# Kernel tuning notes

Hardware: AMD Instinct MI355X
Metric: run time of the kernel (lower is better)

## Reference

```python
import jax, jax.numpy as jnp
import numpy as np

N_RAYS = 65536   # 256x256 image
N_PTS = 128      # samples per ray
FEAT = 3         # RGB
FAR_DELTA = 1e10 # sentinel delta for last sample, as in the torch module


def setup_inputs() -> dict:
    key = jax.random.key(0)
    k1, k2, k3 = jax.random.split(key, 3)
    # depths along each ray must be increasing (deltas computed by diff)
    depth_values = jnp.sort(
        jax.random.uniform(k1, (N_RAYS, N_PTS), jnp.float32, 2.0, 6.0), axis=-1)
    density = jax.random.uniform(k2, (N_RAYS, N_PTS), jnp.float32)  # non-negative
    feature = jax.random.uniform(k3, (N_RAYS, N_PTS, FEAT), jnp.float32)
    return {"depth_values": depth_values, "density": density, "feature": feature}


def reference(depth_values, density, feature):
    n_rays, n_pts = depth_values.shape
    # deltas: consecutive depth differences, huge value appended for last bin
    deltas = jnp.concatenate(
        [depth_values[:, 1:] - depth_values[:, :-1],
         jnp.full((n_rays, 1), FAR_DELTA, depth_values.dtype)], axis=-1)
    tau = density * deltas                              # [n_rays, n_pts]
    # transmittance T_i = exp(-sum_{j<i} tau_j) (exclusive cumsum in log space)
    log_T = -jnp.concatenate(
        [jnp.zeros((n_rays, 1), tau.dtype), jnp.cumsum(tau[:, :-1], axis=-1)],
        axis=-1)
    weights = jnp.exp(log_T) * (1.0 - jnp.exp(-tau))    # [n_rays, n_pts]
    feat_out = jnp.einsum('np,npf->nf', weights, feature)         # [n_rays, F]
    depth_out = jnp.sum(weights * depth_values, axis=-1, keepdims=True)
    return jnp.concatenate([feat_out, depth_out], axis=-1)        # [n_rays, F+1]
```

## Files before the change

kernel.cpp:

```cpp
#include <hip/hip_runtime.h>

#define N_RAYS 65536
#define N_PTS 128
#define FEAT 3
#define FAR_DELTA 1e10f

__global__ __launch_bounds__(256) void volrend_kernel(
    const float* __restrict__ depth,
    const float* __restrict__ density,
    const float* __restrict__ feature,
    float* __restrict__ out)
{
    const int wave = threadIdx.x >> 6;
    const int lane = threadIdx.x & 63;
    const int seg  = lane >> 5;
    const int s    = lane & 31;
    const int base = (blockIdx.x * 4 + wave) * 4;

    const int rayA = base + seg;
    const int rayB = base + 2 + seg;

    const float4 dA = *(const float4*)(depth   + rayA * N_PTS + 4 * s);
    const float4 rA = *(const float4*)(density + rayA * N_PTS + 4 * s);
    const float4 dB = *(const float4*)(depth   + rayB * N_PTS + 4 * s);
    const float4 rB = *(const float4*)(density + rayB * N_PTS + 4 * s);
    const float4* fA = (const float4*)(feature + (size_t)rayA * (N_PTS * FEAT)) + 3 * s;
    const float4* fB = (const float4*)(feature + (size_t)rayB * (N_PTS * FEAT)) + 3 * s;
    const float4 fA0 = fA[0], fA1 = fA[1], fA2 = fA[2];
    const float4 fB0 = fB[0], fB1 = fB[1], fB2 = fB[2];

    float nxA = __shfl_down(dA.x, 1);
    float nxB = __shfl_down(dB.x, 1);
    const bool last = (s == 31);
    float tA0 = rA.x * (dA.y - dA.x);
    float tA1 = rA.y * (dA.z - dA.y);
    float tA2 = rA.z * (dA.w - dA.z);
    float tA3 = rA.w * (last ? FAR_DELTA : (nxA - dA.w));
    float tB0 = rB.x * (dB.y - dB.x);
    float tB1 = rB.y * (dB.z - dB.y);
    float tB2 = rB.z * (dB.w - dB.z);
    float tB3 = rB.w * (last ? FAR_DELTA : (nxB - dB.w));

    float pA = tA0 + tA1 + tA2 + tA3;
    float pB = tB0 + tB1 + tB2 + tB3;
    float eA = __shfl_up(pA, 1, 32);
    float eB = __shfl_up(pB, 1, 32);
    if (s == 0) { eA = 0.0f; eB = 0.0f; }
    #pragma unroll
    for (int off = 1; off < 32; off <<= 1) {
        float xA = __shfl_up(eA, off, 32);
        float xB = __shfl_up(eB, off, 32);
        if (s >= off) { eA += xA; eB += xB; }
    }

    float TA0 = __expf(-eA);
    float TA1 = __expf(-(eA + tA0));
    float TA2 = __expf(-(eA + tA0 + tA1));
    float TA3 = __expf(-(eA + tA0 + tA1 + tA2));
    float TA4 = __expf(-(eA + pA));
    float TB0 = __expf(-eB);
    float TB1 = __expf(-(eB + tB0));
    float TB2 = __expf(-(eB + tB0 + tB1));
    float TB3 = __expf(-(eB + tB0 + tB1 + tB2));
    float TB4 = __expf(-(eB + pB));
    float wA0 = TA0 - TA1, wA1 = TA1 - TA2, wA2 = TA2 - TA3, wA3 = TA3 - TA4;
    float wB0 = TB0 - TB1, wB1 = TB1 - TB2, wB2 = TB2 - TB3, wB3 = TB3 - TB4;

    float a0 = wA0 * fA0.x + wA1 * fA0.w + wA2 * fA1.z + wA3 * fA2.y;
    float a1 = wA0 * fA0.y + wA1 * fA1.x + wA2 * fA1.w + wA3 * fA2.z;
    float a2 = wA0 * fA0.z + wA1 * fA1.y + wA2 * fA2.x + wA3 * fA2.w;
    float a3 = wA0 * dA.x  + wA1 * dA.y  + wA2 * dA.z  + wA3 * dA.w;
    float b0 = wB0 * fB0.x + wB1 * fB0.w + wB2 * fB1.z + wB3 * fB2.y;
    float b1 = wB0 * fB0.y + wB1 * fB1.x + wB2 * fB1.w + wB3 * fB2.z;
    float b2 = wB0 * fB0.z + wB1 * fB1.y + wB2 * fB2.x + wB3 * fB2.w;
    float b3 = wB0 * dB.x  + wB1 * dB.y  + wB2 * dB.z  + wB3 * dB.w;

    #pragma unroll
    for (int off = 16; off > 0; off >>= 1) {
        a0 += __shfl_down(a0, off, 32);
        a1 += __shfl_down(a1, off, 32);
        a2 += __shfl_down(a2, off, 32);
        a3 += __shfl_down(a3, off, 32);
        b0 += __shfl_down(b0, off, 32);
        b1 += __shfl_down(b1, off, 32);
        b2 += __shfl_down(b2, off, 32);
        b3 += __shfl_down(b3, off, 32);
    }

    if (s == 0) {
        *(float4*)(out + (size_t)rayA * 4) = make_float4(a0, a1, a2, a3);
        *(float4*)(out + (size_t)rayB * 4) = make_float4(b0, b1, b2, b3);
    }
}

extern "C" void kernel_launch(void* const* d_in, const int* in_sizes, int n_in,
                              void* d_out, int out_size, void* d_ws, size_t ws_size,
                              hipStream_t stream) {
    const float* depth   = (const float*)d_in[0];
    const float* density = (const float*)d_in[1];
    const float* feature = (const float*)d_in[2];
    float* out = (float*)d_out;

    dim3 grid(N_RAYS / 16);
    dim3 block(256);
    volrend_kernel<<<grid, block, 0, stream>>>(depth, density, feature, out);
}
```

Before: 190.1 us.

## Process multiple ray tiles per block with register prefetch of next tile

Each block now processes four groups of 16 rays in a loop, loading the next group's depth, density and feature vectors into registers before computing and storing the current group. This is meant to keep more memory requests in flight per wave and hide global load latency. It raises register pressure and cuts the grid to a quarter of the blocks, which may lower occupancy or parallelism.

```diff
diff --git a/kernel.cpp b/kernel.cpp
--- a/kernel.cpp
+++ b/kernel.cpp
@@ -4,42 +4,45 @@
 #define N_PTS 128
 #define FEAT 3
 #define FAR_DELTA 1e10f
+#define ITERS 4
+#define RAYS_PER_ITER 16
+#define RAYS_PER_BLOCK (RAYS_PER_ITER * ITERS)
 
-__global__ __launch_bounds__(256) void volrend_kernel(
-    const float* __restrict__ depth,
-    const float* __restrict__ density,
-    const float* __restrict__ feature,
-    float* __restrict__ out)
-{
-    const int wave = threadIdx.x >> 6;
-    const int lane = threadIdx.x & 63;
-    const int seg  = lane >> 5;
-    const int s    = lane & 31;
-    const int base = (blockIdx.x * 4 + wave) * 4;
 
-    const int rayA = base + seg;
-    const int rayB = base + 2 + seg;
+struct Tile {
+    float4 dA, rA, dB, rB;
+    float4 fA0, fA1, fA2, fB0, fB1, fB2;
+};
 
-    const float4 dA = *(const float4*)(depth   + rayA * N_PTS + 4 * s);
-    const float4 rA = *(const float4*)(density + rayA * N_PTS + 4 * s);
-    const float4 dB = *(const float4*)(depth   + rayB * N_PTS + 4 * s);
-    const float4 rB = *(const float4*)(density + rayB * N_PTS + 4 * s);
+__device__ __forceinline__ Tile load_tile(const float* __restrict__ depth,
+                                          const float* __restrict__ density,
+                                          const float* __restrict__ feature,
+                                          int rayA, int rayB, int s) {
+    Tile t;
+    t.dA = *(const float4*)(depth   + (size_t)rayA * N_PTS + 4 * s);
+    t.rA = *(const float4*)(density + (size_t)rayA * N_PTS + 4 * s);
+    t.dB = *(const float4*)(depth   + (size_t)rayB * N_PTS + 4 * s);
+    t.rB = *(const float4*)(density + (size_t)rayB * N_PTS + 4 * s);
     const float4* fA = (const float4*)(feature + (size_t)rayA * (N_PTS * FEAT)) + 3 * s;
     const float4* fB = (const float4*)(feature + (size_t)rayB * (N_PTS * FEAT)) + 3 * s;
-    const float4 fA0 = fA[0], fA1 = fA[1], fA2 = fA[2];
-    const float4 fB0 = fB[0], fB1 = fB[1], fB2 = fB[2];
+    t.fA0 = fA[0]; t.fA1 = fA[1]; t.fA2 = fA[2];
+    t.fB0 = fB[0]; t.fB1 = fB[1]; t.fB2 = fB[2];
+    return t;
+}
 
-    float nxA = __shfl_down(dA.x, 1);
-    float nxB = __shfl_down(dB.x, 1);
+__device__ __forceinline__ void compute_store(const Tile& t, int rayA, int rayB,
+                                              int s, float* __restrict__ out) {
+    float nxA = __shfl_down(t.dA.x, 1);
+    float nxB = __shfl_down(t.dB.x, 1);
     const bool last = (s == 31);
-    float tA0 = rA.x * (dA.y - dA.x);
-    float tA1 = rA.y * (dA.z - dA.y);
-    float tA2 = rA.z * (dA.w - dA.z);
-    float tA3 = rA.w * (last ? FAR_DELTA : (nxA - dA.w));
-    float tB0 = rB.x * (dB.y - dB.x);
-    float tB1 = rB.y * (dB.z - dB.y);
-    float tB2 = rB.z * (dB.w - dB.z);
-    float tB3 = rB.w * (last ? FAR_DELTA : (nxB - dB.w));
+    float tA0 = t.rA.x * (t.dA.y - t.dA.x);
+    float tA1 = t.rA.y * (t.dA.z - t.dA.y);
+    float tA2 = t.rA.z * (t.dA.w - t.dA.z);
+    float tA3 = t.rA.w * (last ? FAR_DELTA : (nxA - t.dA.w));
+    float tB0 = t.rB.x * (t.dB.y - t.dB.x);
+    float tB1 = t.rB.y * (t.dB.z - t.dB.y);
+    float tB2 = t.rB.z * (t.dB.w - t.dB.z);
+    float tB3 = t.rB.w * (last ? FAR_DELTA : (nxB - t.dB.w));
 
     float pA = tA0 + tA1 + tA2 + tA3;
     float pB = tB0 + tB1 + tB2 + tB3;
@@ -66,14 +69,14 @@
     float wA0 = TA0 - TA1, wA1 = TA1 - TA2, wA2 = TA2 - TA3, wA3 = TA3 - TA4;
     float wB0 = TB0 - TB1, wB1 = TB1 - TB2, wB2 = TB2 - TB3, wB3 = TB3 - TB4;
 
-    float a0 = wA0 * fA0.x + wA1 * fA0.w + wA2 * fA1.z + wA3 * fA2.y;
-    float a1 = wA0 * fA0.y + wA1 * fA1.x + wA2 * fA1.w + wA3 * fA2.z;
-    float a2 = wA0 * fA0.z + wA1 * fA1.y + wA2 * fA2.x + wA3 * fA2.w;
-    float a3 = wA0 * dA.x  + wA1 * dA.y  + wA2 * dA.z  + wA3 * dA.w;
-    float b0 = wB0 * fB0.x + wB1 * fB0.w + wB2 * fB1.z + wB3 * fB2.y;
-    float b1 = wB0 * fB0.y + wB1 * fB1.x + wB2 * fB1.w + wB3 * fB2.z;
-    float b2 = wB0 * fB0.z + wB1 * fB1.y + wB2 * fB2.x + wB3 * fB2.w;
-    float b3 = wB0 * dB.x  + wB1 * dB.y  + wB2 * dB.z  + wB3 * dB.w;
+    float a0 = wA0 * t.fA0.x + wA1 * t.fA0.w + wA2 * t.fA1.z + wA3 * t.fA2.y;
+    float a1 = wA0 * t.fA0.y + wA1 * t.fA1.x + wA2 * t.fA1.w + wA3 * t.fA2.z;
+    float a2 = wA0 * t.fA0.z + wA1 * t.fA1.y + wA2 * t.fA2.x + wA3 * t.fA2.w;
+    float a3 = wA0 * t.dA.x  + wA1 * t.dA.y  + wA2 * t.dA.z  + wA3 * t.dA.w;
+    float b0 = wB0 * t.fB0.x + wB1 * t.fB0.w + wB2 * t.fB1.z + wB3 * t.fB2.y;
+    float b1 = wB0 * t.fB0.y + wB1 * t.fB1.x + wB2 * t.fB1.w + wB3 * t.fB2.z;
+    float b2 = wB0 * t.fB0.z + wB1 * t.fB1.y + wB2 * t.fB2.x + wB3 * t.fB2.w;
+    float b3 = wB0 * t.dB.x  + wB1 * t.dB.y  + wB2 * t.dB.z  + wB3 * t.dB.w;
 
     #pragma unroll
     for (int off = 16; off > 0; off >>= 1) {
@@ -93,6 +96,36 @@
     }
 }
 
+__global__ __launch_bounds__(256) void volrend_kernel(
+    const float* __restrict__ depth,
+    const float* __restrict__ density,
+    const float* __restrict__ feature,
+    float* __restrict__ out)
+{
+    const int wv  = threadIdx.x >> 6;
+    const int ln  = threadIdx.x & 63;
+    const int seg = ln >> 5;
+    const int s   = ln & 31;
+
+    const int base  = blockIdx.x * RAYS_PER_BLOCK + wv * 4 + seg;
+    const int rayA0 = base;
+    const int rayB0 = base + 2;
+
+    Tile t = load_tile(depth, density, feature, rayA0, rayB0, s);
+    #pragma unroll
+    for (int i = 0; i < ITERS; ++i) {
+        Tile n;
+        if (i + 1 < ITERS) {
+            n = load_tile(depth, density, feature,
+                          rayA0 + (i + 1) * RAYS_PER_ITER,
+                          rayB0 + (i + 1) * RAYS_PER_ITER, s);
+        }
+        compute_store(t, rayA0 + i * RAYS_PER_ITER, rayB0 + i * RAYS_PER_ITER,
+                      s, out);
+        if (i + 1 < ITERS) t = n;
+    }
+}
+
 extern "C" void kernel_launch(void* const* d_in, const int* in_sizes, int n_in,
                               void* d_out, int out_size, void* d_ws, size_t ws_size,
                               hipStream_t stream) {
@@ -101,7 +134,7 @@
     const float* feature = (const float*)d_in[2];
     float* out = (float*)d_out;
 
-    dim3 grid(N_RAYS / 16);
+    dim3 grid(N_RAYS / RAYS_PER_BLOCK);
     dim3 block(256);
     volrend_kernel<<<grid, block, 0, stream>>>(depth, density, feature, out);
 }
```

Measured after the change: 195.5 us. 1.03x slower.
